# Optimization experiments

Measured on AMD Instinct MI355X. Metric: run time of the kernel, lower is better.

Reference implementation:

```python
import jax, jax.numpy as jnp
import numpy as np

N_NODES = 100000
N_EDGES = 1600000
IN_FEATS = 128
OUT_FEATS = 128


def setup_inputs() -> dict:
    key = jax.random.key(0)
    k1, k2, k3, k4, k5 = jax.random.split(key, 5)
    feat = jax.random.normal(k1, (N_NODES, IN_FEATS), dtype=jnp.float32)
    # He (kaiming) uniform-ish init scale for the weights
    bound = np.sqrt(6.0 / IN_FEATS).astype(np.float32)
    weight_u = jax.random.uniform(k2, (IN_FEATS, OUT_FEATS), jnp.float32, -bound, bound)
    weight_v = jax.random.uniform(k3, (IN_FEATS, OUT_FEATS), jnp.float32, -bound, bound)
    bias = jnp.zeros((OUT_FEATS,), dtype=jnp.float32)
    src = jax.random.randint(k4, (N_EDGES,), 0, N_NODES, dtype=jnp.int32)
    dst = jax.random.randint(k5, (N_EDGES,), 0, N_NODES, dtype=jnp.int32)
    return {"feat": feat, "weight_u": weight_u, "weight_v": weight_v,
            "bias": bias, "src": src, "dst": dst}


def reference(feat, weight_u, weight_v, bias, src, dst):
    n = feat.shape[0]
    # in_feats (128) is not > out_feats (128) -> aggregate first, then matmul
    # m_i = sum_{j in N(i)} h_j  (copy_u + sum over edges)
    agg = jax.ops.segment_sum(feat[src], dst, num_segments=n)  # [N, in_feats]
    rst_u = jnp.matmul(agg, weight_u)                          # [N, out_feats]
    rst_v = jnp.matmul(feat, weight_v)                         # [N, out_feats]
    # in-degree normalization, clamped at 1
    deg = jax.ops.segment_sum(jnp.ones_like(dst, dtype=feat.dtype), dst,
                              num_segments=n)
    norm = 1.0 / jnp.maximum(deg, 1.0)                         # [N]
    out = jax.nn.relu(rst_v + norm[:, None] * rst_u + bias)
    return out
```

## Files before the change

kernel.cpp:

```cpp
#include <hip/hip_runtime.h>
#include <hip/hip_bf16.h>
#include <stdint.h>

#define NN 100000
#define NE 1600000
#define NF 128
#define NTILE ((NN + 63) / 64)
#define GEMM_G 782
#define B_BKT 1563
#define NB2 128
#define EPB (NE / NB2)
#define NCNT (B_BKT * NB2)
#define SC2A ((NCNT + 255) / 256)
#define CONV4 (NN * NF / 4)
#define CONV_BLK ((CONV4 + 255) / 256)
#define SETUP_GRID (NB2 + 16 + CONV_BLK)

typedef __attribute__((ext_vector_type(8))) __bf16 bf16x8;
typedef __attribute__((ext_vector_type(4))) float floatx4;
typedef __attribute__((ext_vector_type(4))) unsigned short ushortx4;
typedef __attribute__((ext_vector_type(8))) unsigned short ushortx8;

static __device__ __forceinline__ unsigned short f2bf(float x) {
    union { float f; unsigned u; } v; v.f = x;
    unsigned r = v.u + 0x7fffu + ((v.u >> 16) & 1u);
    return (unsigned short)(r >> 16);
}
static __device__ __forceinline__ float bflo(unsigned w) {
    union { unsigned u; float f; } v; v.u = w << 16; return v.f;
}
static __device__ __forceinline__ float bfhi(unsigned w) {
    union { unsigned u; float f; } v; v.u = w & 0xffff0000u; return v.f;
}

__global__ void k_setup(const float* __restrict__ feat, unsigned short* __restrict__ featb,
                        const float* __restrict__ wv, const float* __restrict__ wu,
                        unsigned short* __restrict__ w2t,
                        const int* __restrict__ dst, int* __restrict__ counts) {
    __shared__ int h[B_BKT];
    int b = blockIdx.x;
    int tid = threadIdx.x;
    if (b < NB2) {
        for (int i = tid; i < B_BKT; i += 256) h[i] = 0;
        __syncthreads();
        int base = b * EPB, end = base + EPB;
        for (int i = base + tid; i < end; i += 256) {
            int d = __builtin_nontemporal_load(&dst[i]);
            atomicAdd(&h[d >> 6], 1);
        }
        __syncthreads();
        for (int i = tid; i < B_BKT; i += 256)
            counts[i * NB2 + b] = h[i];
    } else if (b < NB2 + 16) {
        int id = (b - NB2) * 256 + tid;
        if (id < 128 * 32) {
            int n = id >> 5, kg = id & 31;
            const float* srcm = (kg < 16) ? wv : wu;
            int k0 = (kg & 15) * 8;
            ushortx8 o;
#pragma unroll
            for (int j = 0; j < 8; ++j)
                o[j] = f2bf(srcm[(k0 + j) * 128 + n]);
            int dchunk = n * 32 + (kg ^ (n & 7));
            *(ushortx8*)(w2t + dchunk * 8) = o;
        }
    } else {
        int i = (b - NB2 - 16) * 256 + tid;
        if (i < CONV4) {
            floatx4 f = __builtin_nontemporal_load((const floatx4*)feat + i);
            ushortx4 o;
            o.x = f2bf(f.x); o.y = f2bf(f.y); o.z = f2bf(f.z); o.w = f2bf(f.w);
            __builtin_nontemporal_store(o, (ushortx4*)featb + i);
        }
    }
}

__global__ void k_scan2_a(int* __restrict__ counts, int* __restrict__ bsums) {
    __shared__ int sh[256];
    int i = blockIdx.x * 256 + threadIdx.x;
    int v = (i < NCNT) ? counts[i] : 0;
    sh[threadIdx.x] = v;
    __syncthreads();
    for (int off = 1; off < 256; off <<= 1) {
        int u = (threadIdx.x >= off) ? sh[threadIdx.x - off] : 0;
        __syncthreads();
        sh[threadIdx.x] += u;
        __syncthreads();
    }
    if (i < NCNT) counts[i] = sh[threadIdx.x] - v;
    if (threadIdx.x == 255) bsums[blockIdx.x] = sh[255];
}
__global__ void k_scan2_b(int* __restrict__ bsums) {
    __shared__ int sh[1024];
    int t = threadIdx.x;
    int v = (t < SC2A) ? bsums[t] : 0;
    sh[t] = v;
    __syncthreads();
    for (int off = 1; off < 1024; off <<= 1) {
        int u = (t >= off) ? sh[t - off] : 0;
        __syncthreads();
        sh[t] += u;
        __syncthreads();
    }
    if (t < SC2A) bsums[t] = sh[t] - v;
}

__global__ void k_binscatter(const int* __restrict__ src, const int* __restrict__ dst,
                             const int* __restrict__ counts, const int* __restrict__ bsums,
                             unsigned* __restrict__ streams) {
    __shared__ int cur[B_BKT];
    int tid = threadIdx.x;
    for (int i = tid; i < B_BKT; i += 512) {
        int idx = i * NB2 + blockIdx.x;
        cur[i] = counts[idx] + bsums[idx >> 8];
    }
    __syncthreads();
    int base = blockIdx.x * EPB, end = base + EPB;
    for (int i = base + tid; i < end; i += 512) {
        int d = __builtin_nontemporal_load(&dst[i]);
        int s = __builtin_nontemporal_load(&src[i]);
        int b = d >> 6;
        unsigned packed = ((unsigned)(d & 63) << 17) | (unsigned)s;
        int pos = atomicAdd(&cur[b], 1);
        streams[pos] = packed;
    }
}

__global__ void k_csr(const unsigned* __restrict__ streams,
                      const int* __restrict__ counts, const int* __restrict__ bsums,
                      int* __restrict__ offs, int* __restrict__ csr) {
    __shared__ int hist[64];
    __shared__ int nodeoff[65];
    int tid = threadIdx.x;
    int bkt = blockIdx.x;
    int idx = bkt * NB2;
    int s = counts[idx] + bsums[idx >> 8];
    int e = (bkt == B_BKT - 1) ? NE : (counts[idx + NB2] + bsums[(idx + NB2) >> 8]);
    if (tid < 64) hist[tid] = 0;
    __syncthreads();
    for (int i = s + tid; i < e; i += 256)
        atomicAdd(&hist[streams[i] >> 17], 1);
    __syncthreads();
    if (tid == 0) {
        int run = 0;
#pragma unroll
        for (int n = 0; n < 64; ++n) { nodeoff[n] = run; run += hist[n]; }
        nodeoff[64] = run;
    }
    __syncthreads();
    if (tid < 64) {
        int node = bkt * 64 + tid;
        if (node < NN) offs[node] = s + nodeoff[tid];
        hist[tid] = nodeoff[tid];
    }
    if (bkt == B_BKT - 1 && tid == 0) offs[NN] = NE;
    __syncthreads();
    for (int i = s + tid; i < e; i += 256) {
        unsigned v = streams[i];
        int p = atomicAdd(&hist[v >> 17], 1);
        csr[s + p] = (int)(v & 0x1FFFFu);
    }
}

__global__ void k_aggregate(const unsigned short* __restrict__ featb,
                            const int* __restrict__ offs,
                            const int* __restrict__ csr,
                            unsigned short* __restrict__ aggb) {
    int lane = threadIdx.x & 63;
    int node = blockIdx.x * 4 + (threadIdx.x >> 6);
    if (node >= NN) return;
    int s0 = offs[node], s1 = offs[node + 1];
    float a0 = 0.f, a1 = 0.f;
    for (int base = s0; base < s1; base += 64) {
        int e = (base + lane < s1) ? csr[base + lane] : 0;
        int m = s1 - base; if (m > 64) m = 64;
        int j = 0;
        for (; j + 8 <= m; j += 8) {
            unsigned w0 = *(const unsigned*)(featb + (size_t)__shfl(e, j + 0, 64) * NF + lane * 2);
            unsigned w1 = *(const unsigned*)(featb + (size_t)__shfl(e, j + 1, 64) * NF + lane * 2);
            unsigned w2 = *(const unsigned*)(featb + (size_t)__shfl(e, j + 2, 64) * NF + lane * 2);
            unsigned w3 = *(const unsigned*)(featb + (size_t)__shfl(e, j + 3, 64) * NF + lane * 2);
            unsigned w4 = *(const unsigned*)(featb + (size_t)__shfl(e, j + 4, 64) * NF + lane * 2);
            unsigned w5 = *(const unsigned*)(featb + (size_t)__shfl(e, j + 5, 64) * NF + lane * 2);
            unsigned w6 = *(const unsigned*)(featb + (size_t)__shfl(e, j + 6, 64) * NF + lane * 2);
            unsigned w7 = *(const unsigned*)(featb + (size_t)__shfl(e, j + 7, 64) * NF + lane * 2);
            a0 += bflo(w0) + bflo(w1) + bflo(w2) + bflo(w3)
                + bflo(w4) + bflo(w5) + bflo(w6) + bflo(w7);
            a1 += bfhi(w0) + bfhi(w1) + bfhi(w2) + bfhi(w3)
                + bfhi(w4) + bfhi(w5) + bfhi(w6) + bfhi(w7);
        }
        for (; j < m; ++j) {
            int nn = __shfl(e, j, 64);
            unsigned w = *(const unsigned*)(featb + (size_t)nn * NF + lane * 2);
            a0 += bflo(w); a1 += bfhi(w);
        }
    }
    int dg = s1 - s0; if (dg < 1) dg = 1;
    float scale = 1.0f / (float)dg;
    unsigned outw = ((unsigned)f2bf(a1 * scale) << 16) | (unsigned)f2bf(a0 * scale);
    *(unsigned*)(aggb + (size_t)node * NF + lane * 2) = outw;
}

static __device__ __forceinline__ void gemm_tile(
    const unsigned short* lds, const bf16x8* a, const float* bsv,
    int rb, int quad, int l15, float* __restrict__ out) {
    floatx4 acc[8];
#pragma unroll
    for (int ct = 0; ct < 8; ++ct) acc[ct] = (floatx4){0.f, 0.f, 0.f, 0.f};
#pragma unroll
    for (int ct = 0; ct < 8; ++ct) {
        int n = ct * 16 + l15;
        int rowoff = n << 8;
        int sw = n & 7;
#pragma unroll
        for (int ks = 0; ks < 8; ++ks) {
            int kg = ks * 4 + quad;
            bf16x8 b = *(const bf16x8*)(&lds[rowoff + ((kg ^ sw) << 3)]);
            acc[ct] = __builtin_amdgcn_mfma_f32_16x16x32_bf16(a[ks], b, acc[ct], 0, 0, 0);
        }
    }
#pragma unroll
    for (int r = 0; r < 4; ++r) {
        int row = rb + quad * 4 + r;
        if (row < NN) {
#pragma unroll
            for (int ct = 0; ct < 8; ++ct) {
                int col = ct * 16 + l15;
                float v = acc[ct][r] + bsv[ct];
                out[(size_t)row * NF + col] = v > 0.f ? v : 0.f;
            }
        }
    }
}

__global__ __launch_bounds__(256, 2) void k_gemm(
    const unsigned short* __restrict__ featb,
    const unsigned short* __restrict__ aggb,
    const unsigned short* __restrict__ w2t,
    const float* __restrict__ bias,
    float* __restrict__ out) {
    __shared__ unsigned short lds[128 * 256];
    for (int i = threadIdx.x; i < 4096; i += 256) {
        ushortx8 w = *(const ushortx8*)(w2t + i * 8);
        *(ushortx8*)(&lds[i * 8]) = w;
    }
    __syncthreads();

    int lane = threadIdx.x & 63;
    int wave = threadIdx.x >> 6;
    int quad = lane >> 4, l15 = lane & 15;

    float bsv[8];
#pragma unroll
    for (int ct = 0; ct < 8; ++ct) bsv[ct] = bias[ct * 16 + l15];

    int t0 = blockIdx.x;
    int t1 = t0 + GEMM_G;
    int t1v = (t1 < NTILE) ? t1 : t0;

    int rb0 = t0 * 64 + wave * 16;
    int rb1 = t1v * 64 + wave * 16;
    int ar0 = rb0 + l15; if (ar0 > NN - 1) ar0 = NN - 1;
    int ar1 = rb1 + l15; if (ar1 > NN - 1) ar1 = NN - 1;
    const unsigned short* fr0 = featb + (size_t)ar0 * NF;
    const unsigned short* ag0 = aggb + (size_t)ar0 * NF;
    const unsigned short* fr1 = featb + (size_t)ar1 * NF;
    const unsigned short* ag1 = aggb + (size_t)ar1 * NF;

    bf16x8 a0[8], a1[8];
#pragma unroll
    for (int ks = 0; ks < 4; ++ks) {
        a0[ks]     = *(const bf16x8*)(fr0 + ks * 32 + quad * 8);
        a0[4 + ks] = *(const bf16x8*)(ag0 + ks * 32 + quad * 8);
    }
#pragma unroll
    for (int ks = 0; ks < 4; ++ks) {
        a1[ks]     = *(const bf16x8*)(fr1 + ks * 32 + quad * 8);
        a1[4 + ks] = *(const bf16x8*)(ag1 + ks * 32 + quad * 8);
    }

    gemm_tile(lds, a0, bsv, rb0, quad, l15, out);
    if (t1 < NTILE)
        gemm_tile(lds, a1, bsv, rb1, quad, l15, out);
}

extern "C" void kernel_launch(void* const* d_in, const int* in_sizes, int n_in,
                              void* d_out, int out_size, void* d_ws, size_t ws_size,
                              hipStream_t stream) {
    const float* feat = (const float*)d_in[0];
    const float* wu   = (const float*)d_in[1];
    const float* wv   = (const float*)d_in[2];
    const float* bias = (const float*)d_in[3];
    const int* src    = (const int*)d_in[4];
    const int* dst    = (const int*)d_in[5];
    float* out        = (float*)d_out;

    char* ws = (char*)d_ws;
    int* counts           = (int*)(ws + 0);
    int* bsums            = (int*)(ws + 800256);
    int* offs             = (int*)(ws + 804352);
    int* csr              = (int*)(ws + 1204480);
    unsigned short* featb = (unsigned short*)(ws + 7604480);
    unsigned short* aggb  = (unsigned short*)(ws + 33204480);
    unsigned short* w2t   = (unsigned short*)(ws + 58804480);
    unsigned* streams     = (unsigned*)aggb;

    k_setup<<<SETUP_GRID, 256, 0, stream>>>(feat, featb, wv, wu, w2t, dst, counts);
    k_scan2_a<<<SC2A, 256, 0, stream>>>(counts, bsums);
    k_scan2_b<<<1, 1024, 0, stream>>>(bsums);
    k_binscatter<<<NB2, 512, 0, stream>>>(src, dst, counts, bsums, streams);
    k_csr<<<B_BKT, 256, 0, stream>>>(streams, counts, bsums, offs, csr);
    k_aggregate<<<(NN + 3) / 4, 256, 0, stream>>>(featb, offs, csr, aggb);
    k_gemm<<<GEMM_G, 256, 0, stream>>>(featb, aggb, w2t, bias, out);
}
```

Before: 295.1 us.

## Fuse CSR build into aggregation via LDS bucket sort and restructure GEMM epilogue

Merges the CSR-construction kernel and the aggregation kernel into one. Each bucket block sorts its edges into shared memory and then aggregates its 64 nodes directly, so the global CSR and offset arrays are never written or re-read. A slow scan fallback handles buckets larger than the shared-memory capacity. The GEMM now computes each tile transposed by swapping the MFMA operands, so each lane writes float4 outputs. It runs 512 blocks with up to four tiles each and prefetches the next tile's A rows. Aggregation parallelism drops from 25k blocks to 1563 blocks of four waves, each handling 16 nodes serially, which may reduce latency hiding.

```diff
diff --git a/kernel.cpp b/kernel.cpp
--- a/kernel.cpp
+++ b/kernel.cpp
@@ -6,7 +6,7 @@
 #define NE 1600000
 #define NF 128
 #define NTILE ((NN + 63) / 64)
-#define GEMM_G 782
+#define GEMM_BLKS 512
 #define B_BKT 1563
 #define NB2 128
 #define EPB (NE / NB2)
@@ -15,6 +15,7 @@
 #define CONV4 (NN * NF / 4)
 #define CONV_BLK ((CONV4 + 255) / 256)
 #define SETUP_GRID (NB2 + 16 + CONV_BLK)
+#define CAP 3072
 
 typedef __attribute__((ext_vector_type(8))) __bf16 bf16x8;
 typedef __attribute__((ext_vector_type(4))) float floatx4;
@@ -126,16 +127,21 @@
     }
 }
 
-__global__ void k_csr(const unsigned* __restrict__ streams,
-                      const int* __restrict__ counts, const int* __restrict__ bsums,
-                      int* __restrict__ offs, int* __restrict__ csr) {
+__global__ void k_aggsort(const unsigned* __restrict__ streams,
+                          const int* __restrict__ counts, const int* __restrict__ bsums,
+                          const unsigned short* __restrict__ featb,
+                          unsigned short* __restrict__ aggb) {
     __shared__ int hist[64];
     __shared__ int nodeoff[65];
+    __shared__ int eb[CAP];
     int tid = threadIdx.x;
     int bkt = blockIdx.x;
     int idx = bkt * NB2;
     int s = counts[idx] + bsums[idx >> 8];
     int e = (bkt == B_BKT - 1) ? NE : (counts[idx + NB2] + bsums[(idx + NB2) >> 8]);
+    int seg = e - s;
+    int lane = tid & 63, wave = tid >> 6;
+
     if (tid < 64) hist[tid] = 0;
     __syncthreads();
     for (int i = s + tid; i < e; i += 256)
@@ -148,61 +154,74 @@
         nodeoff[64] = run;
     }
     __syncthreads();
-    if (tid < 64) {
-        int node = bkt * 64 + tid;
-        if (node < NN) offs[node] = s + nodeoff[tid];
-        hist[tid] = nodeoff[tid];
-    }
-    if (bkt == B_BKT - 1 && tid == 0) offs[NN] = NE;
-    __syncthreads();
-    for (int i = s + tid; i < e; i += 256) {
-        unsigned v = streams[i];
-        int p = atomicAdd(&hist[v >> 17], 1);
-        csr[s + p] = (int)(v & 0x1FFFFu);
-    }
-}
-
-__global__ void k_aggregate(const unsigned short* __restrict__ featb,
-                            const int* __restrict__ offs,
-                            const int* __restrict__ csr,
-                            unsigned short* __restrict__ aggb) {
-    int lane = threadIdx.x & 63;
-    int node = blockIdx.x * 4 + (threadIdx.x >> 6);
-    if (node >= NN) return;
-    int s0 = offs[node], s1 = offs[node + 1];
-    float a0 = 0.f, a1 = 0.f;
-    for (int base = s0; base < s1; base += 64) {
-        int e = (base + lane < s1) ? csr[base + lane] : 0;
-        int m = s1 - base; if (m > 64) m = 64;
-        int j = 0;
-        for (; j + 8 <= m; j += 8) {
-            unsigned w0 = *(const unsigned*)(featb + (size_t)__shfl(e, j + 0, 64) * NF + lane * 2);
-            unsigned w1 = *(const unsigned*)(featb + (size_t)__shfl(e, j + 1, 64) * NF + lane * 2);
-            unsigned w2 = *(const unsigned*)(featb + (size_t)__shfl(e, j + 2, 64) * NF + lane * 2);
-            unsigned w3 = *(const unsigned*)(featb + (size_t)__shfl(e, j + 3, 64) * NF + lane * 2);
-            unsigned w4 = *(const unsigned*)(featb + (size_t)__shfl(e, j + 4, 64) * NF + lane * 2);
-            unsigned w5 = *(const unsigned*)(featb + (size_t)__shfl(e, j + 5, 64) * NF + lane * 2);
-            unsigned w6 = *(const unsigned*)(featb + (size_t)__shfl(e, j + 6, 64) * NF + lane * 2);
-            unsigned w7 = *(const unsigned*)(featb + (size_t)__shfl(e, j + 7, 64) * NF + lane * 2);
-            a0 += bflo(w0) + bflo(w1) + bflo(w2) + bflo(w3)
-                + bflo(w4) + bflo(w5) + bflo(w6) + bflo(w7);
-            a1 += bfhi(w0) + bfhi(w1) + bfhi(w2) + bfhi(w3)
-                + bfhi(w4) + bfhi(w5) + bfhi(w6) + bfhi(w7);
-        }
-        for (; j < m; ++j) {
-            int nn = __shfl(e, j, 64);
-            unsigned w = *(const unsigned*)(featb + (size_t)nn * NF + lane * 2);
-            a0 += bflo(w); a1 += bfhi(w);
-        }
-    }
-    int dg = s1 - s0; if (dg < 1) dg = 1;
-    float scale = 1.0f / (float)dg;
-    unsigned outw = ((unsigned)f2bf(a1 * scale) << 16) | (unsigned)f2bf(a0 * scale);
-    *(unsigned*)(aggb + (size_t)node * NF + lane * 2) = outw;
-}
-
-static __device__ __forceinline__ void gemm_tile(
-    const unsigned short* lds, const bf16x8* a, const float* bsv,
+    if (tid < 64) hist[tid] = nodeoff[tid];
+    __syncthreads();
+
+    if (seg <= CAP) {
+        for (int i = s + tid; i < e; i += 256) {
+            unsigned v = streams[i];
+            int p = atomicAdd(&hist[v >> 17], 1);
+            eb[p] = (int)(v & 0x1FFFFu);
+        }
+        __syncthreads();
+        for (int nl = wave * 16; nl < wave * 16 + 16; ++nl) {
+            int node = bkt * 64 + nl;
+            if (node >= NN) break;
+            int s0 = nodeoff[nl], s1 = nodeoff[nl + 1];
+            float a0 = 0.f, a1 = 0.f;
+            for (int base = s0; base < s1; base += 64) {
+                int ee = (base + lane < s1) ? eb[base + lane] : 0;
+                int m = s1 - base; if (m > 64) m = 64;
+                int j = 0;
+                for (; j + 8 <= m; j += 8) {
+                    unsigned w0 = *(const unsigned*)(featb + (size_t)__shfl(ee, j + 0, 64) * NF + lane * 2);
+                    unsigned w1 = *(const unsigned*)(featb + (size_t)__shfl(ee, j + 1, 64) * NF + lane * 2);
+                    unsigned w2 = *(const unsigned*)(featb + (size_t)__shfl(ee, j + 2, 64) * NF + lane * 2);
+                    unsigned w3 = *(const unsigned*)(featb + (size_t)__shfl(ee, j + 3, 64) * NF + lane * 2);
+                    unsigned w4 = *(const unsigned*)(featb + (size_t)__shfl(ee, j + 4, 64) * NF + lane * 2);
+                    unsigned w5 = *(const unsigned*)(featb + (size_t)__shfl(ee, j + 5, 64) * NF + lane * 2);
+                    unsigned w6 = *(const unsigned*)(featb + (size_t)__shfl(ee, j + 6, 64) * NF + lane * 2);
+                    unsigned w7 = *(const unsigned*)(featb + (size_t)__shfl(ee, j + 7, 64) * NF + lane * 2);
+                    a0 += bflo(w0) + bflo(w1) + bflo(w2) + bflo(w3)
+                        + bflo(w4) + bflo(w5) + bflo(w6) + bflo(w7);
+                    a1 += bfhi(w0) + bfhi(w1) + bfhi(w2) + bfhi(w3)
+                        + bfhi(w4) + bfhi(w5) + bfhi(w6) + bfhi(w7);
+                }
+                for (; j < m; ++j) {
+                    int nn = __shfl(ee, j, 64);
+                    unsigned w = *(const unsigned*)(featb + (size_t)nn * NF + lane * 2);
+                    a0 += bflo(w); a1 += bfhi(w);
+                }
+            }
+            int dg = s1 - s0; if (dg < 1) dg = 1;
+            float scale = 1.0f / (float)dg;
+            unsigned outw = ((unsigned)f2bf(a1 * scale) << 16) | (unsigned)f2bf(a0 * scale);
+            *(unsigned*)(aggb + (size_t)node * NF + lane * 2) = outw;
+        }
+    } else {
+        for (int nl = wave * 16; nl < wave * 16 + 16; ++nl) {
+            int node = bkt * 64 + nl;
+            if (node >= NN) break;
+            float a0 = 0.f, a1 = 0.f;
+            int dg = 0;
+            for (int i = s; i < e; ++i) {
+                unsigned v = streams[i];
+                if ((int)(v >> 17) == nl) {
+                    ++dg;
+                    unsigned w = *(const unsigned*)(featb + (size_t)(v & 0x1FFFFu) * NF + lane * 2);
+                    a0 += bflo(w); a1 += bfhi(w);
+                }
+            }
+            int dc = dg < 1 ? 1 : dg;
+            float scale = 1.0f / (float)dc;
+            unsigned outw = ((unsigned)f2bf(a1 * scale) << 16) | (unsigned)f2bf(a0 * scale);
+            *(unsigned*)(aggb + (size_t)node * NF + lane * 2) = outw;
+        }
+    }
+}
+
+static __device__ __forceinline__ void gemm_tile_sw(
+    const unsigned short* lds, const bf16x8* a, const float* __restrict__ bias,
     int rb, int quad, int l15, float* __restrict__ out) {
     floatx4 acc[8];
 #pragma unroll
@@ -216,22 +235,38 @@
         for (int ks = 0; ks < 8; ++ks) {
             int kg = ks * 4 + quad;
             bf16x8 b = *(const bf16x8*)(&lds[rowoff + ((kg ^ sw) << 3)]);
-            acc[ct] = __builtin_amdgcn_mfma_f32_16x16x32_bf16(a[ks], b, acc[ct], 0, 0, 0);
-        }
-    }
-#pragma unroll
-    for (int r = 0; r < 4; ++r) {
-        int row = rb + quad * 4 + r;
-        if (row < NN) {
-#pragma unroll
-            for (int ct = 0; ct < 8; ++ct) {
-                int col = ct * 16 + l15;
-                float v = acc[ct][r] + bsv[ct];
-                out[(size_t)row * NF + col] = v > 0.f ? v : 0.f;
-            }
-        }
-    }
-}
+            acc[ct] = __builtin_amdgcn_mfma_f32_16x16x32_bf16(b, a[ks], acc[ct], 0, 0, 0);
+        }
+    }
+    int row = rb + l15;
+    if (row < NN) {
+        float* orow = out + (size_t)row * NF;
+#pragma unroll
+        for (int ct = 0; ct < 8; ++ct) {
+            floatx4 bv = *(const floatx4*)(bias + ct * 16 + quad * 4);
+            floatx4 v;
+            v.x = acc[ct].x + bv.x; v.y = acc[ct].y + bv.y;
+            v.z = acc[ct].z + bv.z; v.w = acc[ct].w + bv.w;
+            v.x = v.x > 0.f ? v.x : 0.f;
+            v.y = v.y > 0.f ? v.y : 0.f;
+            v.z = v.z > 0.f ? v.z : 0.f;
+            v.w = v.w > 0.f ? v.w : 0.f;
+            *(floatx4*)(orow + ct * 16 + quad * 4) = v;
+        }
+    }
+}
+
+#define LOADA(A, rb)                                                          \
+    {                                                                         \
+        int ar = (rb) + l15; if (ar > NN - 1) ar = NN - 1;                    \
+        const unsigned short* fr = featb + (size_t)ar * NF;                   \
+        const unsigned short* ag = aggb + (size_t)ar * NF;                    \
+        _Pragma("unroll")                                                     \
+        for (int ks = 0; ks < 4; ++ks) {                                      \
+            A[ks]     = *(const bf16x8*)(fr + ks * 32 + quad * 8);            \
+            A[4 + ks] = *(const bf16x8*)(ag + ks * 32 + quad * 8);            \
+        }                                                                     \
+    }
 
 __global__ __launch_bounds__(256, 2) void k_gemm(
     const unsigned short* __restrict__ featb,
@@ -250,38 +285,25 @@
     int wave = threadIdx.x >> 6;
     int quad = lane >> 4, l15 = lane & 15;
 
-    float bsv[8];
-#pragma unroll
-    for (int ct = 0; ct < 8; ++ct) bsv[ct] = bias[ct * 16 + l15];
-
     int t0 = blockIdx.x;
-    int t1 = t0 + GEMM_G;
-    int t1v = (t1 < NTILE) ? t1 : t0;
-
+    int t1 = t0 + GEMM_BLKS, t2 = t0 + 2 * GEMM_BLKS, t3 = t0 + 3 * GEMM_BLKS;
+    bool has3 = (t3 < NTILE);
     int rb0 = t0 * 64 + wave * 16;
-    int rb1 = t1v * 64 + wave * 16;
-    int ar0 = rb0 + l15; if (ar0 > NN - 1) ar0 = NN - 1;
-    int ar1 = rb1 + l15; if (ar1 > NN - 1) ar1 = NN - 1;
-    const unsigned short* fr0 = featb + (size_t)ar0 * NF;
-    const unsigned short* ag0 = aggb + (size_t)ar0 * NF;
-    const unsigned short* fr1 = featb + (size_t)ar1 * NF;
-    const unsigned short* ag1 = aggb + (size_t)ar1 * NF;
-
-    bf16x8 a0[8], a1[8];
-#pragma unroll
-    for (int ks = 0; ks < 4; ++ks) {
-        a0[ks]     = *(const bf16x8*)(fr0 + ks * 32 + quad * 8);
-        a0[4 + ks] = *(const bf16x8*)(ag0 + ks * 32 + quad * 8);
-    }
-#pragma unroll
-    for (int ks = 0; ks < 4; ++ks) {
-        a1[ks]     = *(const bf16x8*)(fr1 + ks * 32 + quad * 8);
-        a1[4 + ks] = *(const bf16x8*)(ag1 + ks * 32 + quad * 8);
-    }
-
-    gemm_tile(lds, a0, bsv, rb0, quad, l15, out);
-    if (t1 < NTILE)
-        gemm_tile(lds, a1, bsv, rb1, quad, l15, out);
+    int rb1 = t1 * 64 + wave * 16;
+    int rb2 = t2 * 64 + wave * 16;
+
+    bf16x8 A0[8], A1[8], A2[8];
+    LOADA(A0, rb0);
+    LOADA(A1, rb1);
+    LOADA(A2, rb2);
+
+    gemm_tile_sw(lds, A0, bias, rb0, quad, l15, out);
+    int rb3 = t3 * 64 + wave * 16;
+    if (has3) LOADA(A0, rb3);
+    gemm_tile_sw(lds, A1, bias, rb1, quad, l15, out);
+    gemm_tile_sw(lds, A2, bias, rb2, quad, l15, out);
+    if (has3)
+        gemm_tile_sw(lds, A0, bias, rb3, quad, l15, out);
 }
 
 extern "C" void kernel_launch(void* const* d_in, const int* in_sizes, int n_in,
@@ -298,18 +320,15 @@
     char* ws = (char*)d_ws;
     int* counts           = (int*)(ws + 0);
     int* bsums            = (int*)(ws + 800256);
-    int* offs             = (int*)(ws + 804352);
-    int* csr              = (int*)(ws + 1204480);
+    unsigned* streams     = (unsigned*)(ws + 1204480);
     unsigned short* featb = (unsigned short*)(ws + 7604480);
     unsigned short* aggb  = (unsigned short*)(ws + 33204480);
     unsigned short* w2t   = (unsigned short*)(ws + 58804480);
-    unsigned* streams     = (unsigned*)aggb;
 
     k_setup<<<SETUP_GRID, 256, 0, stream>>>(feat, featb, wv, wu, w2t, dst, counts);
     k_scan2_a<<<SC2A, 256, 0, stream>>>(counts, bsums);
     k_scan2_b<<<1, 1024, 0, stream>>>(bsums);
     k_binscatter<<<NB2, 512, 0, stream>>>(src, dst, counts, bsums, streams);
-    k_csr<<<B_BKT, 256, 0, stream>>>(streams, counts, bsums, offs, csr);
-    k_aggregate<<<(NN + 3) / 4, 256, 0, stream>>>(featb, offs, csr, aggb);
-    k_gemm<<<GEMM_G, 256, 0, stream>>>(featb, aggb, w2t, bias, out);
-}
+    k_aggsort<<<B_BKT, 256, 0, stream>>>(streams, counts, bsums, featb, aggb);
+    k_gemm<<<GEMM_BLKS, 256, 0, stream>>>(featb, aggb, w2t, bias, out);
+}
```

Result: slower. 305.8 us (+3.6%).

## Fuse CSR build and aggregation into one per-bucket kernel using LDS edge buffer

Applied to the files above, without the earlier changes.

Merges the CSR construction and neighbor aggregation kernels: each 64-node bucket sorts its edges into shared memory and then its waves pull nodes dynamically and gather feature rows directly. This removes the global offs/csr write and reread and one kernel launch. The streams buffer moves to its own workspace region because aggb is now written while streams is still being read. Buckets with more than CAP edges fall back to a slow linear scan per node. The fused kernel runs only 1563 blocks with 12KB of LDS each, so the gather phase may get less parallelism than the old per-node launch.

```diff
diff --git a/kernel.cpp b/kernel.cpp
--- a/kernel.cpp
+++ b/kernel.cpp
@@ -15,6 +15,7 @@
 #define CONV4 (NN * NF / 4)
 #define CONV_BLK ((CONV4 + 255) / 256)
 #define SETUP_GRID (NB2 + 16 + CONV_BLK)
+#define CAP 3072
 
 typedef __attribute__((ext_vector_type(8))) __bf16 bf16x8;
 typedef __attribute__((ext_vector_type(4))) float floatx4;
@@ -126,17 +127,24 @@
     }
 }
 
-__global__ void k_csr(const unsigned* __restrict__ streams,
-                      const int* __restrict__ counts, const int* __restrict__ bsums,
-                      int* __restrict__ offs, int* __restrict__ csr) {
+__global__ void k_aggsort(const unsigned* __restrict__ streams,
+                          const int* __restrict__ counts, const int* __restrict__ bsums,
+                          const unsigned short* __restrict__ featb,
+                          unsigned short* __restrict__ aggb) {
     __shared__ int hist[64];
     __shared__ int nodeoff[65];
+    __shared__ int eb[CAP];
+    __shared__ int nextn;
     int tid = threadIdx.x;
     int bkt = blockIdx.x;
     int idx = bkt * NB2;
     int s = counts[idx] + bsums[idx >> 8];
     int e = (bkt == B_BKT - 1) ? NE : (counts[idx + NB2] + bsums[(idx + NB2) >> 8]);
+    int seg = e - s;
+    int lane = tid & 63, wave = tid >> 6;
+
     if (tid < 64) hist[tid] = 0;
+    if (tid == 0) nextn = 0;
     __syncthreads();
     for (int i = s + tid; i < e; i += 256)
         atomicAdd(&hist[streams[i] >> 17], 1);
@@ -148,57 +156,74 @@
         nodeoff[64] = run;
     }
     __syncthreads();
-    if (tid < 64) {
-        int node = bkt * 64 + tid;
-        if (node < NN) offs[node] = s + nodeoff[tid];
-        hist[tid] = nodeoff[tid];
-    }
-    if (bkt == B_BKT - 1 && tid == 0) offs[NN] = NE;
-    __syncthreads();
-    for (int i = s + tid; i < e; i += 256) {
-        unsigned v = streams[i];
-        int p = atomicAdd(&hist[v >> 17], 1);
-        csr[s + p] = (int)(v & 0x1FFFFu);
-    }
-}
-
-__global__ void k_aggregate(const unsigned short* __restrict__ featb,
-                            const int* __restrict__ offs,
-                            const int* __restrict__ csr,
-                            unsigned short* __restrict__ aggb) {
-    int lane = threadIdx.x & 63;
-    int node = blockIdx.x * 4 + (threadIdx.x >> 6);
-    if (node >= NN) return;
-    int s0 = offs[node], s1 = offs[node + 1];
-    float a0 = 0.f, a1 = 0.f;
-    for (int base = s0; base < s1; base += 64) {
-        int e = (base + lane < s1) ? csr[base + lane] : 0;
-        int m = s1 - base; if (m > 64) m = 64;
-        int j = 0;
-        for (; j + 8 <= m; j += 8) {
-            unsigned w0 = *(const unsigned*)(featb + (size_t)__shfl(e, j + 0, 64) * NF + lane * 2);
-            unsigned w1 = *(const unsigned*)(featb + (size_t)__shfl(e, j + 1, 64) * NF + lane * 2);
-            unsigned w2 = *(const unsigned*)(featb + (size_t)__shfl(e, j + 2, 64) * NF + lane * 2);
-            unsigned w3 = *(const unsigned*)(featb + (size_t)__shfl(e, j + 3, 64) * NF + lane * 2);
-            unsigned w4 = *(const unsigned*)(featb + (size_t)__shfl(e, j + 4, 64) * NF + lane * 2);
-            unsigned w5 = *(const unsigned*)(featb + (size_t)__shfl(e, j + 5, 64) * NF + lane * 2);
-            unsigned w6 = *(const unsigned*)(featb + (size_t)__shfl(e, j + 6, 64) * NF + lane * 2);
-            unsigned w7 = *(const unsigned*)(featb + (size_t)__shfl(e, j + 7, 64) * NF + lane * 2);
-            a0 += bflo(w0) + bflo(w1) + bflo(w2) + bflo(w3)
-                + bflo(w4) + bflo(w5) + bflo(w6) + bflo(w7);
-            a1 += bfhi(w0) + bfhi(w1) + bfhi(w2) + bfhi(w3)
-                + bfhi(w4) + bfhi(w5) + bfhi(w6) + bfhi(w7);
-        }
-        for (; j < m; ++j) {
-            int nn = __shfl(e, j, 64);
-            unsigned w = *(const unsigned*)(featb + (size_t)nn * NF + lane * 2);
-            a0 += bflo(w); a1 += bfhi(w);
-        }
-    }
-    int dg = s1 - s0; if (dg < 1) dg = 1;
-    float scale = 1.0f / (float)dg;
-    unsigned outw = ((unsigned)f2bf(a1 * scale) << 16) | (unsigned)f2bf(a0 * scale);
-    *(unsigned*)(aggb + (size_t)node * NF + lane * 2) = outw;
+    if (tid < 64) hist[tid] = nodeoff[tid];
+    __syncthreads();
+
+    if (seg <= CAP) {
+        for (int i = s + tid; i < e; i += 256) {
+            unsigned v = streams[i];
+            int p = atomicAdd(&hist[v >> 17], 1);
+            eb[p] = (int)(v & 0x1FFFFu);
+        }
+        __syncthreads();
+        for (;;) {
+            int nl;
+            if (lane == 0) nl = atomicAdd(&nextn, 1);
+            nl = __shfl(nl, 0, 64);
+            if (nl >= 64) break;
+            int node = bkt * 64 + nl;
+            if (node >= NN) continue;
+            int s0 = nodeoff[nl], s1 = nodeoff[nl + 1];
+            float a0 = 0.f, a1 = 0.f;
+            for (int base = s0; base < s1; base += 64) {
+                int ee = (base + lane < s1) ? eb[base + lane] : 0;
+                int m = s1 - base; if (m > 64) m = 64;
+                int j = 0;
+                for (; j + 8 <= m; j += 8) {
+                    unsigned w0 = *(const unsigned*)(featb + (size_t)__shfl(ee, j + 0, 64) * NF + lane * 2);
+                    unsigned w1 = *(const unsigned*)(featb + (size_t)__shfl(ee, j + 1, 64) * NF + lane * 2);
+                    unsigned w2 = *(const unsigned*)(featb + (size_t)__shfl(ee, j + 2, 64) * NF + lane * 2);
+                    unsigned w3 = *(const unsigned*)(featb + (size_t)__shfl(ee, j + 3, 64) * NF + lane * 2);
+                    unsigned w4 = *(const unsigned*)(featb + (size_t)__shfl(ee, j + 4, 64) * NF + lane * 2);
+                    unsigned w5 = *(const unsigned*)(featb + (size_t)__shfl(ee, j + 5, 64) * NF + lane * 2);
+                    unsigned w6 = *(const unsigned*)(featb + (size_t)__shfl(ee, j + 6, 64) * NF + lane * 2);
+                    unsigned w7 = *(const unsigned*)(featb + (size_t)__shfl(ee, j + 7, 64) * NF + lane * 2);
+                    a0 += bflo(w0) + bflo(w1) + bflo(w2) + bflo(w3)
+                        + bflo(w4) + bflo(w5) + bflo(w6) + bflo(w7);
+                    a1 += bfhi(w0) + bfhi(w1) + bfhi(w2) + bfhi(w3)
+                        + bfhi(w4) + bfhi(w5) + bfhi(w6) + bfhi(w7);
+                }
+                for (; j < m; ++j) {
+                    int nn = __shfl(ee, j, 64);
+                    unsigned w = *(const unsigned*)(featb + (size_t)nn * NF + lane * 2);
+                    a0 += bflo(w); a1 += bfhi(w);
+                }
+            }
+            int dg = s1 - s0; if (dg < 1) dg = 1;
+            float scale = 1.0f / (float)dg;
+            unsigned outw = ((unsigned)f2bf(a1 * scale) << 16) | (unsigned)f2bf(a0 * scale);
+            *(unsigned*)(aggb + (size_t)node * NF + lane * 2) = outw;
+        }
+    } else {
+        for (int nl = wave * 16; nl < wave * 16 + 16; ++nl) {
+            int node = bkt * 64 + nl;
+            if (node >= NN) break;
+            float a0 = 0.f, a1 = 0.f;
+            int dg = 0;
+            for (int i = s; i < e; ++i) {
+                unsigned v = streams[i];
+                if ((int)(v >> 17) == nl) {
+                    ++dg;
+                    unsigned w = *(const unsigned*)(featb + (size_t)(v & 0x1FFFFu) * NF + lane * 2);
+                    a0 += bflo(w); a1 += bfhi(w);
+                }
+            }
+            int dc = dg < 1 ? 1 : dg;
+            float scale = 1.0f / (float)dc;
+            unsigned outw = ((unsigned)f2bf(a1 * scale) << 16) | (unsigned)f2bf(a0 * scale);
+            *(unsigned*)(aggb + (size_t)node * NF + lane * 2) = outw;
+        }
+    }
 }
 
 static __device__ __forceinline__ void gemm_tile(
@@ -298,18 +323,15 @@
     char* ws = (char*)d_ws;
     int* counts           = (int*)(ws + 0);
     int* bsums            = (int*)(ws + 800256);
-    int* offs             = (int*)(ws + 804352);
-    int* csr              = (int*)(ws + 1204480);
+    unsigned* streams     = (unsigned*)(ws + 1204480);
     unsigned short* featb = (unsigned short*)(ws + 7604480);
     unsigned short* aggb  = (unsigned short*)(ws + 33204480);
     unsigned short* w2t   = (unsigned short*)(ws + 58804480);
-    unsigned* streams     = (unsigned*)aggb;
 
     k_setup<<<SETUP_GRID, 256, 0, stream>>>(feat, featb, wv, wu, w2t, dst, counts);
     k_scan2_a<<<SC2A, 256, 0, stream>>>(counts, bsums);
     k_scan2_b<<<1, 1024, 0, stream>>>(bsums);
     k_binscatter<<<NB2, 512, 0, stream>>>(src, dst, counts, bsums, streams);
-    k_csr<<<B_BKT, 256, 0, stream>>>(streams, counts, bsums, offs, csr);
-    k_aggregate<<<(NN + 3) / 4, 256, 0, stream>>>(featb, offs, csr, aggb);
+    k_aggsort<<<B_BKT, 256, 0, stream>>>(streams, counts, bsums, featb, aggb);
     k_gemm<<<GEMM_G, 256, 0, stream>>>(featb, aggb, w2t, bias, out);
 }
```

Measured after the change: 287.7 us. 2.5% less time.
